# Kernel optimization log

Measured on AMD Instinct MI355X. Metric: run time of the kernel, lower is better.

The kernel has to match this reference:

```python
import jax, jax.numpy as jnp
import numpy as np

N_NODES = 10000
N_EDGES = 320000
FIN = 2
HID = 64
OUT = 16
B = 4
T = 12


def _gcn_norm(src, dst, w, n):
    # add self loops (fill value 1.0, improved=False), then symmetric normalization
    loop = jnp.arange(n, dtype=src.dtype)
    src = jnp.concatenate([src, loop])
    dst = jnp.concatenate([dst, loop])
    w = jnp.concatenate([w, jnp.ones((n,), w.dtype)])
    deg = jax.ops.segment_sum(w, dst, num_segments=n)
    dinv = jnp.where(deg > 0, 1.0 / jnp.sqrt(deg), 0.0)
    return src, dst, dinv[src] * w * dinv[dst]


def _gcn_conv(x_nbf, src, dst, norm, W, b, n):
    # x_nbf: [N,B,F] ; GCNConv: (x W) aggregated with normalized weights, + bias
    xw = jnp.einsum('nbf,fh->nbh', x_nbf, W)          # [N,B,H]
    msgs = xw[src] * norm[:, None, None]               # [E',B,H]
    return jax.ops.segment_sum(msgs, dst, num_segments=n) + b


def setup_inputs() -> dict:
    key = jax.random.key(0)
    ks = jax.random.split(key, 20)
    x = jax.random.normal(ks[0], (B, N_NODES, FIN, T), jnp.float32)
    edge_index = jax.random.randint(ks[1], (2, N_EDGES), 0, N_NODES, jnp.int64 if jax.config.jax_enable_x64 else jnp.int32)
    edge_weight = jax.random.uniform(ks[2], (N_EDGES,), jnp.float32)
    s = 0.1
    p = {
        'Wz': s * jax.random.normal(ks[3], (FIN, HID), jnp.float32),
        'bz': jnp.zeros((HID,), jnp.float32),
        'Wr': s * jax.random.normal(ks[4], (FIN, HID), jnp.float32),
        'br': jnp.zeros((HID,), jnp.float32),
        'Wh': s * jax.random.normal(ks[5], (FIN, HID), jnp.float32),
        'bh': jnp.zeros((HID,), jnp.float32),
        'Lz_w': s * jax.random.normal(ks[6], (2 * HID, HID), jnp.float32),
        'Lz_b': jnp.zeros((HID,), jnp.float32),
        'Lr_w': s * jax.random.normal(ks[7], (2 * HID, HID), jnp.float32),
        'Lr_b': jnp.zeros((HID,), jnp.float32),
        'Lh_w': s * jax.random.normal(ks[8], (2 * HID, HID), jnp.float32),
        'Lh_b': jnp.zeros((HID,), jnp.float32),
        'lin_w': s * jax.random.normal(ks[9], (HID, OUT), jnp.float32),
        'lin_b': jnp.zeros((OUT,), jnp.float32),
    }
    return dict(x=x, edge_index=edge_index, edge_weight=edge_weight, **p)


def reference(x, edge_index, edge_weight, Wz, bz, Wr, br, Wh, bh,
              Lz_w, Lz_b, Lr_w, Lr_b, Lh_w, Lh_b, lin_w, lin_b):
    Bd, N, Fin, Td = x.shape
    src, dst, norm = _gcn_norm(edge_index[0], edge_index[1], edge_weight, N)
    H0 = jnp.zeros((N, Bd, Wz.shape[1]), x.dtype)
    xs = jnp.transpose(x, (3, 1, 0, 2))  # [T,N,B,Fin]

    def step(H, xt):
        cz = _gcn_conv(xt, src, dst, norm, Wz, bz, N)
        Z = jax.nn.sigmoid(jnp.concatenate([cz, H], -1) @ Lz_w + Lz_b)
        cr = _gcn_conv(xt, src, dst, norm, Wr, br, N)
        R = jax.nn.sigmoid(jnp.concatenate([cr, H], -1) @ Lr_w + Lr_b)
        ch = _gcn_conv(xt, src, dst, norm, Wh, bh, N)
        H_tilde = jnp.tanh(jnp.concatenate([ch, H * R], -1) @ Lh_w + Lh_b)
        Hn = Z * H + (1.0 - Z) * H_tilde
        out_t = jax.nn.relu(Hn) @ lin_w + lin_b  # [N,B,OUT]
        return Hn, out_t

    _, outs = jax.lax.scan(step, H0, xs)        # [T,N,B,OUT]
    return jnp.transpose(outs, (2, 0, 1, 3))     # [B,T,N,OUT]
```

## Files before the change

kernel.cpp:

```cpp
#include <hip/hip_runtime.h>
#include <cstdint>
#include <cstddef>

#define NN      10000
#define NE      320000
#define FINF    2
#define HIDN    64
#define OUTN    16
#define BBATCH  4
#define TSTEPS  12
#define NBROWS  (NN * BBATCH)
#define XTN     (TSTEPS * NN * BBATCH * FINF)
#define CAP     96

typedef _Float16 v8h __attribute__((ext_vector_type(8)));
typedef _Float16 v2h __attribute__((ext_vector_type(2)));
typedef float    v4f __attribute__((ext_vector_type(4)));

extern "C" __global__ void setup_kernel(const float* __restrict__ x,
                             const int* __restrict__ src, const int* __restrict__ dst,
                             const float* __restrict__ ew,
                             int* __restrict__ cnt, float* __restrict__ degf,
                             int2* __restrict__ bucket, _Float16* __restrict__ xAll,
                             const float* __restrict__ Wz, const float* __restrict__ bz,
                             const float* __restrict__ Wr, const float* __restrict__ br,
                             const float* __restrict__ Wh, const float* __restrict__ bh,
                             const float* __restrict__ Lz, const float* __restrict__ Lz_b,
                             const float* __restrict__ Lr, const float* __restrict__ Lr_b,
                             const float* __restrict__ Lh, const float* __restrict__ Lh_b,
                             const float* __restrict__ linw, const float* __restrict__ linb,
                             float* __restrict__ PP) {
    int idx = blockIdx.x * 256 + threadIdx.x;
    if (idx < BBATCH * NN) {
        int b = idx / NN;
        int n = idx - b * NN;
        const float* xp = x + (size_t)idx * (FINF * TSTEPS);
        v2h* xo = (v2h*)xAll;
        #pragma unroll
        for (int t = 0; t < TSTEPS; ++t) {
            v2h p;
            p.x = (_Float16)xp[t];
            p.y = (_Float16)xp[TSTEPS + t];
            xo[n * 48 + t * 4 + b] = p;
        }
    }
    if (idx < NE) {
        int d = dst[idx];
        int s = src[idx];
        float w = ew[idx];
        int p = atomicAdd(&cnt[d], 1);
        if (p < CAP) {
            int2 rec;
            rec.x = s;
            rec.y = __float_as_int(w);
            bucket[d * CAP + p] = rec;
        }
        atomicAdd(&degf[d], w);
    }
    if (idx < 13904) {
        const float* Lg[3]    = {Lz, Lr, Lh};
        const float* Lbias[3] = {Lz_b, Lr_b, Lh_b};
        const float* Wg[3]    = {Wz, Wr, Wh};
        const float* bg[3]    = {bz, br, bh};
        int i = idx;
        if (i < 12288) {
            int g = i >> 12, rr = (i >> 6) & 63, j = i & 63;
            PP[i] = Lg[g][(64 + rr) * 64 + j];
        } else if (i < 12672) {
            int i2 = i - 12288;
            int g = i2 >> 7, f = (i2 >> 6) & 1, j = i2 & 63;
            float s = 0.f;
            for (int k = 0; k < 64; ++k) s = fmaf(Wg[g][f * 64 + k], Lg[g][k * 64 + j], s);
            PP[i] = s;
        } else if (i < 12864) {
            int i3 = i - 12672;
            int g = i3 >> 6, j = i3 & 63;
            float s = Lbias[g][j];
            for (int k = 0; k < 64; ++k) s = fmaf(bg[g][k], Lg[g][k * 64 + j], s);
            PP[i] = s;
        } else if (i < 13888) {
            PP[i] = linw[i - 12864];
        } else {
            PP[i] = linb[i - 13888];
        }
    }
}

__device__ __forceinline__ float fsigmoid(float x) {
    return 1.0f / (1.0f + __expf(-x));
}

extern "C" __global__ __launch_bounds__(256, 3)
void fused_kernel(const _Float16* __restrict__ xAll, const int2* __restrict__ bucket,
                  const int* __restrict__ cnt, const float* __restrict__ degf,
                  const float* __restrict__ PP, float* __restrict__ out) {
    __shared__ _Float16 WTH[64 * 72 + 32];
    __shared__ _Float16 WIZR[2 * 64 * 8 + 32];
    __shared__ _Float16 Hm[4][16 * 72];
    __shared__ float    aggL[16 * 96];
    __shared__ int      s_src[16 * CAP];
    __shared__ float    s_c[16 * CAP];
    __shared__ int      s_cnt[16];
    const int tid = threadIdx.x;
    const int w   = tid >> 6;
    const int l   = tid & 63;
    const int m   = l & 15;
    const int q   = l >> 4;
    const int n0  = blockIdx.x * 16 + w * 4 + q;

    {
        const int nl = tid >> 4;
        const int u  = tid & 15;
        const int ng = blockIdx.x * 16 + nl;
        const int c  = min(cnt[ng], CAP);
        if (u == 0) s_cnt[nl] = c;
        const float dn = rsqrtf(1.0f + degf[ng]);
        for (int i = u; i < c; i += 16) {
            int2 rec = bucket[ng * CAP + i];
            int s = rec.x;
            s_src[nl * CAP + i] = s;
            s_c[nl * CAP + i]   = __int_as_float(rec.y) * dn * rsqrtf(1.0f + degf[s]);
        }
    }

    for (int i = tid; i < 4096; i += 256) {
        int k = i >> 6, n = i & 63;
        WTH[n * 72 + k] = (_Float16)PP[8192 + i];
    }
    for (int i = tid; i < 64 * 8; i += 256) {
        int n = i >> 3, kk = i & 7;
        float v = 0.f;
        if (kk == 0)      v = PP[12288 + 2 * 128 + n];
        else if (kk == 1) v = PP[12288 + 2 * 128 + 64 + n];
        else if (kk == 2) v = PP[12672 + 2 * 64 + n];
        WTH[n * 72 + 64 + kk] = (_Float16)v;
    }
    for (int i = tid; i < 32; i += 256) WTH[64 * 72 + i] = (_Float16)0.f;
    for (int i = tid; i < 2 * 64 * 8; i += 256) {
        int g = i >> 9, rem = i & 511, n = rem >> 3, kk = rem & 7;
        float v = 0.f;
        if (kk == 0)      v = PP[12288 + g * 128 + n];
        else if (kk == 1) v = PP[12288 + g * 128 + 64 + n];
        else if (kk == 2) v = PP[12672 + g * 64 + n];
        WIZR[(g * 64 + n) * 8 + kk] = (_Float16)v;
    }
    for (int i = tid; i < 32; i += 256) WIZR[1024 + i] = (_Float16)0.f;

    __syncthreads();

    {
        const int nl = tid >> 4;
        const int u  = tid & 15;
        const int ng = blockIdx.x * 16 + nl;
        const int c  = s_cnt[nl];
        const float dn = rsqrtf(1.0f + degf[ng]);
        const v2h* x2 = (const v2h*)xAll;
        float acc[6];
        {
            v2h a = x2[(size_t)ng * 48 + u * 3];
            v2h b = x2[(size_t)ng * 48 + u * 3 + 1];
            v2h e = x2[(size_t)ng * 48 + u * 3 + 2];
            float c0 = dn * dn;
            acc[0] = c0 * (float)a.x; acc[1] = c0 * (float)a.y;
            acc[2] = c0 * (float)b.x; acc[3] = c0 * (float)b.y;
            acc[4] = c0 * (float)e.x; acc[5] = c0 * (float)e.y;
        }
        for (int i = 0; i < c; ++i) {
            int s    = s_src[nl * CAP + i];
            float cc = s_c[nl * CAP + i];
            v2h a = x2[(size_t)s * 48 + u * 3];
            v2h b = x2[(size_t)s * 48 + u * 3 + 1];
            v2h e = x2[(size_t)s * 48 + u * 3 + 2];
            acc[0] = fmaf(cc, (float)a.x, acc[0]);
            acc[1] = fmaf(cc, (float)a.y, acc[1]);
            acc[2] = fmaf(cc, (float)b.x, acc[2]);
            acc[3] = fmaf(cc, (float)b.y, acc[3]);
            acc[4] = fmaf(cc, (float)e.x, acc[4]);
            acc[5] = fmaf(cc, (float)e.y, acc[5]);
        }
        #pragma unroll
        for (int jj = 0; jj < 6; ++jj) aggL[nl * 96 + u * 6 + jj] = acc[jj];
    }

    v8h BZ[4][2], BR[4][2];
    #pragma unroll
    for (int nt = 0; nt < 4; ++nt) {
        #pragma unroll
        for (int c = 0; c < 2; ++c) {
            #pragma unroll
            for (int i = 0; i < 8; ++i) {
                int k = c * 32 + q * 8 + i;
                BZ[nt][c][i] = (_Float16)PP[k * 64 + nt * 16 + m];
                BR[nt][c][i] = (_Float16)PP[4096 + k * 64 + nt * 16 + m];
            }
        }
    }
    v8h linB0, linB1;
    #pragma unroll
    for (int i = 0; i < 8; ++i) {
        linB0[i] = (_Float16)PP[12864 + (q * 8 + i) * 16 + m];
        linB1[i] = (_Float16)PP[12864 + (32 + q * 8 + i) * 16 + m];
    }
    const float linbv = PP[13888 + m];

    __syncthreads();

    _Float16* __restrict__ Hw = &Hm[w][0];
    const int wsw = (q & 2) << 3;
    const _Float16* __restrict__ Ard = Hw + m * 72 + ((q ^ ((m >> 2) & 2)) * 8);
    const int aggBase = (w * 4 + (m >> 2)) * 96 + (m & 3) * 2;

    float Hold[4][4];
    #pragma unroll
    for (int nt = 0; nt < 4; ++nt)
        #pragma unroll
        for (int r = 0; r < 4; ++r) Hold[nt][r] = 0.f;
    v8h aH0{}, aH1{};

    const v4f zeroc = {0.f, 0.f, 0.f, 0.f};

    for (int t = 0; t < TSTEPS; ++t) {
        v8h aI{};
        if (q == 0) {
            const float2 av = *(const float2*)&aggL[aggBase + t * 8];
            aI[0] = (_Float16)av.x;
            aI[1] = (_Float16)av.y;
            aI[2] = (_Float16)1.0f;
        }

        v4f accZ[4], accR[4];
        #pragma unroll
        for (int nt = 0; nt < 4; ++nt) {
            const v8h bIz = *(const v8h*)&WIZR[(0 * 64 + nt * 16 + m) * 8 + q * 8];
            const v8h bIr = *(const v8h*)&WIZR[(1 * 64 + nt * 16 + m) * 8 + q * 8];
            accZ[nt] = __builtin_amdgcn_mfma_f32_16x16x32_f16(aI,  bIz,       zeroc,    0, 0, 0);
            accZ[nt] = __builtin_amdgcn_mfma_f32_16x16x32_f16(aH0, BZ[nt][0], accZ[nt], 0, 0, 0);
            accZ[nt] = __builtin_amdgcn_mfma_f32_16x16x32_f16(aH1, BZ[nt][1], accZ[nt], 0, 0, 0);
            accR[nt] = __builtin_amdgcn_mfma_f32_16x16x32_f16(aI,  bIr,       zeroc,    0, 0, 0);
            accR[nt] = __builtin_amdgcn_mfma_f32_16x16x32_f16(aH0, BR[nt][0], accR[nt], 0, 0, 0);
            accR[nt] = __builtin_amdgcn_mfma_f32_16x16x32_f16(aH1, BR[nt][1], accR[nt], 0, 0, 0);
        }

        float Z[4][4];
        #pragma unroll
        for (int nt = 0; nt < 4; ++nt) {
            #pragma unroll
            for (int r = 0; r < 4; ++r) {
                Z[nt][r] = fsigmoid(accZ[nt][r]);
                float hr = Hold[nt][r] * fsigmoid(accR[nt][r]);
                Hw[(q * 4 + r) * 72 + ((nt * 16 + m) ^ wsw)] = (_Float16)hr;
            }
        }
        __threadfence_block();
        const v8h aP0 = *(const v8h*)Ard;
        const v8h aP1 = *(const v8h*)(Ard + 32);

        v4f accH[4];
        #pragma unroll
        for (int nt = 0; nt < 4; ++nt) {
            const _Float16* bh = &WTH[(nt * 16 + m) * 72 + q * 8];
            accH[nt] = __builtin_amdgcn_mfma_f32_16x16x32_f16(aI,  *(const v8h*)(bh + 64), zeroc,    0, 0, 0);
            accH[nt] = __builtin_amdgcn_mfma_f32_16x16x32_f16(aP0, *(const v8h*)bh,        accH[nt], 0, 0, 0);
            accH[nt] = __builtin_amdgcn_mfma_f32_16x16x32_f16(aP1, *(const v8h*)(bh + 32), accH[nt], 0, 0, 0);
        }

        #pragma unroll
        for (int nt = 0; nt < 4; ++nt) {
            #pragma unroll
            for (int r = 0; r < 4; ++r) {
                float ht = fmaf(2.0f, fsigmoid(2.0f * accH[nt][r]), -1.0f);
                float hn = Z[nt][r] * Hold[nt][r] + (1.f - Z[nt][r]) * ht;
                Hold[nt][r] = hn;
                Hw[(q * 4 + r) * 72 + ((nt * 16 + m) ^ wsw)] = (_Float16)hn;
            }
        }
        __threadfence_block();
        aH0 = *(const v8h*)Ard;
        aH1 = *(const v8h*)(Ard + 32);

        const v8h zz{};
        v8h r0 = __builtin_elementwise_max(aH0, zz);
        v8h r1 = __builtin_elementwise_max(aH1, zz);
        v4f accO = {linbv, linbv, linbv, linbv};
        accO = __builtin_amdgcn_mfma_f32_16x16x32_f16(r0, linB0, accO, 0, 0, 0);
        accO = __builtin_amdgcn_mfma_f32_16x16x32_f16(r1, linB1, accO, 0, 0, 0);
        #pragma unroll
        for (int r = 0; r < 4; ++r)
            out[(((size_t)r * TSTEPS + t) * NN + n0) * 16 + m] = accO[r];
    }
}


extern "C" void kernel_launch(void* const* d_in, const int* in_sizes, int n_in,
                              void* d_out, int out_size, void* d_ws, size_t ws_size,
                              hipStream_t stream) {
    const float* x   = (const float*)d_in[0];
    const int*   ei  = (const int*)d_in[1];
    const float* ew  = (const float*)d_in[2];
    const float* Wz  = (const float*)d_in[3];
    const float* bz  = (const float*)d_in[4];
    const float* Wr  = (const float*)d_in[5];
    const float* br  = (const float*)d_in[6];
    const float* Wh  = (const float*)d_in[7];
    const float* bh  = (const float*)d_in[8];
    const float* Lz  = (const float*)d_in[9];
    const float* Lz_b= (const float*)d_in[10];
    const float* Lr  = (const float*)d_in[11];
    const float* Lr_b= (const float*)d_in[12];
    const float* Lh  = (const float*)d_in[13];
    const float* Lh_b= (const float*)d_in[14];
    const float* lw  = (const float*)d_in[15];
    const float* lb  = (const float*)d_in[16];
    float* out = (float*)d_out;

    char* ws = (char*)d_ws;
    size_t off = 0;
    auto alloc = [&](size_t bytes) -> char* {
        char* p = ws + off;
        off += (bytes + 15) & ~(size_t)15;
        return p;
    };
    _Float16* xAll = (_Float16*)alloc((size_t)XTN * 2);
    float* PP      = (float*)alloc(13904 * 4);
    int2*  bucket  = (int2*) alloc((size_t)NN * CAP * 8);
    int*   cnt     = (int*)  alloc(NN * 4);
    float* degf    = (float*)alloc(NN * 4);

    const int* srcp = ei;
    const int* dstp = ei + NE;

    hipMemsetAsync(cnt, 0, 2 * NN * sizeof(int), stream);
    setup_kernel<<<(NE + 255) / 256, 256, 0, stream>>>(x, srcp, dstp, ew, cnt, degf,
                                                       bucket, xAll,
                                                       Wz, bz, Wr, br, Wh, bh,
                                                       Lz, Lz_b, Lr, Lr_b, Lh, Lh_b,
                                                       lw, lb, PP);
    fused_kernel<<<NN / 16, 256, 0, stream>>>(xAll, bucket, cnt, degf, PP, out);
}
```

Measured before the change: 221.2 us.

## Split hidden columns across wave pairs and halve nodes per block

New measurement: 224.6 us. About the same (+1.5%).

```diff
diff --git a/kernel.cpp b/kernel.cpp
--- a/kernel.cpp
+++ b/kernel.cpp
@@ -90,28 +90,31 @@
     return 1.0f / (1.0f + __expf(-x));
 }
 
-extern "C" __global__ __launch_bounds__(256, 3)
+extern "C" __global__ __launch_bounds__(256, 5)
 void fused_kernel(const _Float16* __restrict__ xAll, const int2* __restrict__ bucket,
                   const int* __restrict__ cnt, const float* __restrict__ degf,
                   const float* __restrict__ PP, float* __restrict__ out) {
     __shared__ _Float16 WTH[64 * 72 + 32];
     __shared__ _Float16 WIZR[2 * 64 * 8 + 32];
-    __shared__ _Float16 Hm[4][16 * 72];
-    __shared__ float    aggL[16 * 96];
-    __shared__ int      s_src[16 * CAP];
-    __shared__ float    s_c[16 * CAP];
-    __shared__ int      s_cnt[16];
+    __shared__ _Float16 HA[2][16 * 72];
+    __shared__ _Float16 HB[2][16 * 72];
+    __shared__ float    aggL[8 * 96];
+    __shared__ int      s_src[8 * CAP];
+    __shared__ float    s_c[8 * CAP];
+    __shared__ int      s_cnt[8];
     const int tid = threadIdx.x;
     const int w   = tid >> 6;
     const int l   = tid & 63;
     const int m   = l & 15;
     const int q   = l >> 4;
-    const int n0  = blockIdx.x * 16 + w * 4 + q;
-
-    {
+    const int rt  = w >> 1;
+    const int ch  = w & 1;
+    const int n0  = blockIdx.x * 8 + rt * 4 + q;
+
+    if (tid < 128) {
         const int nl = tid >> 4;
         const int u  = tid & 15;
-        const int ng = blockIdx.x * 16 + nl;
+        const int ng = blockIdx.x * 8 + nl;
         const int c  = min(cnt[ng], CAP);
         if (u == 0) s_cnt[nl] = c;
         const float dn = rsqrtf(1.0f + degf[ng]);
@@ -121,37 +124,60 @@
             s_src[nl * CAP + i] = s;
             s_c[nl * CAP + i]   = __int_as_float(rec.y) * dn * rsqrtf(1.0f + degf[s]);
         }
-    }
-
-    for (int i = tid; i < 4096; i += 256) {
-        int k = i >> 6, n = i & 63;
-        WTH[n * 72 + k] = (_Float16)PP[8192 + i];
-    }
-    for (int i = tid; i < 64 * 8; i += 256) {
-        int n = i >> 3, kk = i & 7;
-        float v = 0.f;
-        if (kk == 0)      v = PP[12288 + 2 * 128 + n];
-        else if (kk == 1) v = PP[12288 + 2 * 128 + 64 + n];
-        else if (kk == 2) v = PP[12672 + 2 * 64 + n];
-        WTH[n * 72 + 64 + kk] = (_Float16)v;
-    }
-    for (int i = tid; i < 32; i += 256) WTH[64 * 72 + i] = (_Float16)0.f;
-    for (int i = tid; i < 2 * 64 * 8; i += 256) {
-        int g = i >> 9, rem = i & 511, n = rem >> 3, kk = rem & 7;
-        float v = 0.f;
-        if (kk == 0)      v = PP[12288 + g * 128 + n];
-        else if (kk == 1) v = PP[12288 + g * 128 + 64 + n];
-        else if (kk == 2) v = PP[12672 + g * 64 + n];
-        WIZR[(g * 64 + n) * 8 + kk] = (_Float16)v;
-    }
-    for (int i = tid; i < 32; i += 256) WIZR[1024 + i] = (_Float16)0.f;
+    } else {
+        const int t2 = tid - 128;
+        for (int i = t2; i < 4096; i += 128) {
+            int k = i >> 6, n = i & 63;
+            WTH[n * 72 + k] = (_Float16)PP[8192 + i];
+        }
+        for (int i = t2; i < 64 * 8; i += 128) {
+            int n = i >> 3, kk = i & 7;
+            float v = 0.f;
+            if (kk == 0)      v = PP[12288 + 2 * 128 + n];
+            else if (kk == 1) v = PP[12288 + 2 * 128 + 64 + n];
+            else if (kk == 2) v = PP[12672 + 2 * 64 + n];
+            WTH[n * 72 + 64 + kk] = (_Float16)v;
+        }
+        for (int i = t2; i < 32; i += 128) WTH[64 * 72 + i] = (_Float16)0.f;
+        for (int i = t2; i < 2 * 64 * 8; i += 128) {
+            int g = i >> 9, rem = i & 511, n = rem >> 3, kk = rem & 7;
+            float v = 0.f;
+            if (kk == 0)      v = PP[12288 + g * 128 + n];
+            else if (kk == 1) v = PP[12288 + g * 128 + 64 + n];
+            else if (kk == 2) v = PP[12672 + g * 64 + n];
+            WIZR[(g * 64 + n) * 8 + kk] = (_Float16)v;
+        }
+        for (int i = t2; i < 32; i += 128) WIZR[1024 + i] = (_Float16)0.f;
+    }
 
     __syncthreads();
 
-    {
+    v8h BZ[2][2], BR[2][2];
+    #pragma unroll
+    for (int j = 0; j < 2; ++j) {
+        const int nt = ch * 2 + j;
+        #pragma unroll
+        for (int c = 0; c < 2; ++c) {
+            #pragma unroll
+            for (int i = 0; i < 8; ++i) {
+                int k = c * 32 + q * 8 + i;
+                BZ[j][c][i] = (_Float16)PP[k * 64 + nt * 16 + m];
+                BR[j][c][i] = (_Float16)PP[4096 + k * 64 + nt * 16 + m];
+            }
+        }
+    }
+    v8h linB0, linB1;
+    #pragma unroll
+    for (int i = 0; i < 8; ++i) {
+        linB0[i] = (_Float16)PP[12864 + (q * 8 + i) * 16 + m];
+        linB1[i] = (_Float16)PP[12864 + (32 + q * 8 + i) * 16 + m];
+    }
+    const float linbv = PP[13888 + m];
+
+    if (tid < 128) {
         const int nl = tid >> 4;
         const int u  = tid & 15;
-        const int ng = blockIdx.x * 16 + nl;
+        const int ng = blockIdx.x * 8 + nl;
         const int c  = s_cnt[nl];
         const float dn = rsqrtf(1.0f + degf[ng]);
         const v2h* x2 = (const v2h*)xAll;
@@ -182,39 +208,21 @@
         for (int jj = 0; jj < 6; ++jj) aggL[nl * 96 + u * 6 + jj] = acc[jj];
     }
 
-    v8h BZ[4][2], BR[4][2];
+    __syncthreads();
+
+    _Float16* __restrict__ HwA = &HA[rt][0];
+    _Float16* __restrict__ HwB = &HB[rt][0];
+    const int wsw = (q & 2) << 3;
+    const int rdo = (q ^ ((m >> 2) & 2)) * 8;
+    const _Float16* __restrict__ ArdA = HwA + m * 72 + rdo;
+    const _Float16* __restrict__ ArdB = HwB + m * 72 + rdo;
+    const int aggBase = (rt * 4 + (m >> 2)) * 96 + (m & 3) * 2;
+
+    float Hold[2][4];
     #pragma unroll
-    for (int nt = 0; nt < 4; ++nt) {
-        #pragma unroll
-        for (int c = 0; c < 2; ++c) {
-            #pragma unroll
-            for (int i = 0; i < 8; ++i) {
-                int k = c * 32 + q * 8 + i;
-                BZ[nt][c][i] = (_Float16)PP[k * 64 + nt * 16 + m];
-                BR[nt][c][i] = (_Float16)PP[4096 + k * 64 + nt * 16 + m];
-            }
-        }
-    }
-    v8h linB0, linB1;
-    #pragma unroll
-    for (int i = 0; i < 8; ++i) {
-        linB0[i] = (_Float16)PP[12864 + (q * 8 + i) * 16 + m];
-        linB1[i] = (_Float16)PP[12864 + (32 + q * 8 + i) * 16 + m];
-    }
-    const float linbv = PP[13888 + m];
-
-    __syncthreads();
-
-    _Float16* __restrict__ Hw = &Hm[w][0];
-    const int wsw = (q & 2) << 3;
-    const _Float16* __restrict__ Ard = Hw + m * 72 + ((q ^ ((m >> 2) & 2)) * 8);
-    const int aggBase = (w * 4 + (m >> 2)) * 96 + (m & 3) * 2;
-
-    float Hold[4][4];
-    #pragma unroll
-    for (int nt = 0; nt < 4; ++nt)
-        #pragma unroll
-        for (int r = 0; r < 4; ++r) Hold[nt][r] = 0.f;
+    for (int j = 0; j < 2; ++j)
+        #pragma unroll
+        for (int r = 0; r < 4; ++r) Hold[j][r] = 0.f;
     v8h aH0{}, aH1{};
 
     const v4f zeroc = {0.f, 0.f, 0.f, 0.f};
@@ -228,65 +236,70 @@
             aI[2] = (_Float16)1.0f;
         }
 
-        v4f accZ[4], accR[4];
-        #pragma unroll
-        for (int nt = 0; nt < 4; ++nt) {
+        v4f accZ[2], accR[2];
+        #pragma unroll
+        for (int j = 0; j < 2; ++j) {
+            const int nt = ch * 2 + j;
             const v8h bIz = *(const v8h*)&WIZR[(0 * 64 + nt * 16 + m) * 8 + q * 8];
             const v8h bIr = *(const v8h*)&WIZR[(1 * 64 + nt * 16 + m) * 8 + q * 8];
-            accZ[nt] = __builtin_amdgcn_mfma_f32_16x16x32_f16(aI,  bIz,       zeroc,    0, 0, 0);
-            accZ[nt] = __builtin_amdgcn_mfma_f32_16x16x32_f16(aH0, BZ[nt][0], accZ[nt], 0, 0, 0);
-            accZ[nt] = __builtin_amdgcn_mfma_f32_16x16x32_f16(aH1, BZ[nt][1], accZ[nt], 0, 0, 0);
-            accR[nt] = __builtin_amdgcn_mfma_f32_16x16x32_f16(aI,  bIr,       zeroc,    0, 0, 0);
-            accR[nt] = __builtin_amdgcn_mfma_f32_16x16x32_f16(aH0, BR[nt][0], accR[nt], 0, 0, 0);
-            accR[nt] = __builtin_amdgcn_mfma_f32_16x16x32_f16(aH1, BR[nt][1], accR[nt], 0, 0, 0);
-        }
-
-        float Z[4][4];
-        #pragma unroll
-        for (int nt = 0; nt < 4; ++nt) {
+            accZ[j] = __builtin_amdgcn_mfma_f32_16x16x32_f16(aI,  bIz,      zeroc,   0, 0, 0);
+            accZ[j] = __builtin_amdgcn_mfma_f32_16x16x32_f16(aH0, BZ[j][0], accZ[j], 0, 0, 0);
+            accZ[j] = __builtin_amdgcn_mfma_f32_16x16x32_f16(aH1, BZ[j][1], accZ[j], 0, 0, 0);
+            accR[j] = __builtin_amdgcn_mfma_f32_16x16x32_f16(aI,  bIr,      zeroc,   0, 0, 0);
+            accR[j] = __builtin_amdgcn_mfma_f32_16x16x32_f16(aH0, BR[j][0], accR[j], 0, 0, 0);
+            accR[j] = __builtin_amdgcn_mfma_f32_16x16x32_f16(aH1, BR[j][1], accR[j], 0, 0, 0);
+        }
+
+        float Z[2][4];
+        #pragma unroll
+        for (int j = 0; j < 2; ++j) {
+            const int colb = (ch * 2 + j) * 16 + m;
             #pragma unroll
             for (int r = 0; r < 4; ++r) {
-                Z[nt][r] = fsigmoid(accZ[nt][r]);
-                float hr = Hold[nt][r] * fsigmoid(accR[nt][r]);
-                Hw[(q * 4 + r) * 72 + ((nt * 16 + m) ^ wsw)] = (_Float16)hr;
+                Z[j][r] = fsigmoid(accZ[j][r]);
+                float hr = Hold[j][r] * fsigmoid(accR[j][r]);
+                HwA[(q * 4 + r) * 72 + (colb ^ wsw)] = (_Float16)hr;
             }
         }
-        __threadfence_block();
-        const v8h aP0 = *(const v8h*)Ard;
-        const v8h aP1 = *(const v8h*)(Ard + 32);
-
-        v4f accH[4];
-        #pragma unroll
-        for (int nt = 0; nt < 4; ++nt) {
-            const _Float16* bh = &WTH[(nt * 16 + m) * 72 + q * 8];
-            accH[nt] = __builtin_amdgcn_mfma_f32_16x16x32_f16(aI,  *(const v8h*)(bh + 64), zeroc,    0, 0, 0);
-            accH[nt] = __builtin_amdgcn_mfma_f32_16x16x32_f16(aP0, *(const v8h*)bh,        accH[nt], 0, 0, 0);
-            accH[nt] = __builtin_amdgcn_mfma_f32_16x16x32_f16(aP1, *(const v8h*)(bh + 32), accH[nt], 0, 0, 0);
-        }
-
-        #pragma unroll
-        for (int nt = 0; nt < 4; ++nt) {
+        __syncthreads();
+        const v8h aP0 = *(const v8h*)ArdA;
+        const v8h aP1 = *(const v8h*)(ArdA + 32);
+
+        v4f accH[2];
+        #pragma unroll
+        for (int j = 0; j < 2; ++j) {
+            const _Float16* bh = &WTH[((ch * 2 + j) * 16 + m) * 72 + q * 8];
+            accH[j] = __builtin_amdgcn_mfma_f32_16x16x32_f16(aI,  *(const v8h*)(bh + 64), zeroc,   0, 0, 0);
+            accH[j] = __builtin_amdgcn_mfma_f32_16x16x32_f16(aP0, *(const v8h*)bh,        accH[j], 0, 0, 0);
+            accH[j] = __builtin_amdgcn_mfma_f32_16x16x32_f16(aP1, *(const v8h*)(bh + 32), accH[j], 0, 0, 0);
+        }
+
+        #pragma unroll
+        for (int j = 0; j < 2; ++j) {
+            const int colb = (ch * 2 + j) * 16 + m;
             #pragma unroll
             for (int r = 0; r < 4; ++r) {
-                float ht = fmaf(2.0f, fsigmoid(2.0f * accH[nt][r]), -1.0f);
-                float hn = Z[nt][r] * Hold[nt][r] + (1.f - Z[nt][r]) * ht;
-                Hold[nt][r] = hn;
-                Hw[(q * 4 + r) * 72 + ((nt * 16 + m) ^ wsw)] = (_Float16)hn;
+                float ht = fmaf(2.0f, fsigmoid(2.0f * accH[j][r]), -1.0f);
+                float hn = Z[j][r] * Hold[j][r] + (1.f - Z[j][r]) * ht;
+                Hold[j][r] = hn;
+                HwB[(q * 4 + r) * 72 + (colb ^ wsw)] = (_Float16)hn;
             }
         }
-        __threadfence_block();
-        aH0 = *(const v8h*)Ard;
-        aH1 = *(const v8h*)(Ard + 32);
-
-        const v8h zz{};
-        v8h r0 = __builtin_elementwise_max(aH0, zz);
-        v8h r1 = __builtin_elementwise_max(aH1, zz);
-        v4f accO = {linbv, linbv, linbv, linbv};
-        accO = __builtin_amdgcn_mfma_f32_16x16x32_f16(r0, linB0, accO, 0, 0, 0);
-        accO = __builtin_amdgcn_mfma_f32_16x16x32_f16(r1, linB1, accO, 0, 0, 0);
-        #pragma unroll
-        for (int r = 0; r < 4; ++r)
-            out[(((size_t)r * TSTEPS + t) * NN + n0) * 16 + m] = accO[r];
+        __syncthreads();
+        aH0 = *(const v8h*)ArdB;
+        aH1 = *(const v8h*)(ArdB + 32);
+
+        if (ch == (t & 1)) {
+            const v8h zz{};
+            v8h r0 = __builtin_elementwise_max(aH0, zz);
+            v8h r1 = __builtin_elementwise_max(aH1, zz);
+            v4f accO = {linbv, linbv, linbv, linbv};
+            accO = __builtin_amdgcn_mfma_f32_16x16x32_f16(r0, linB0, accO, 0, 0, 0);
+            accO = __builtin_amdgcn_mfma_f32_16x16x32_f16(r1, linB1, accO, 0, 0, 0);
+            #pragma unroll
+            for (int r = 0; r < 4; ++r)
+                out[(((size_t)r * TSTEPS + t) * NN + n0) * 16 + m] = accO[r];
+        }
     }
 }
 
@@ -335,5 +348,5 @@
                                                        Wz, bz, Wr, br, Wh, bh,
                                                        Lz, Lz_b, Lr, Lr_b, Lh, Lh_b,
                                                        lw, lb, PP);
-    fused_kernel<<<NN / 16, 256, 0, stream>>>(xAll, bucket, cnt, degf, PP, out);
+    fused_kernel<<<NN / 8, 256, 0, stream>>>(xAll, bucket, cnt, degf, PP, out);
 }
```
